# Optimization experiments

Hardware: AMD Instinct MI355X
Metric: run time of the kernel (lower is better)

## Reference

```python
import jax, jax.numpy as jnp
import numpy as np

HIDDEN = 512
LAYERS = 3
K = 8
EPS = 1e-5


def build_adjacency(coords, k):
    # squared pairwise distances (monotone in cdist, so same top-k indices)
    sq = jnp.sum(coords * coords, axis=-1)                      # [B,N]
    d2 = sq[:, :, None] + sq[:, None, :] - 2.0 * jnp.einsum('bnc,bmc->bnm', coords, coords)
    _, idx = jax.lax.top_k(-d2, k + 1)                          # smallest k+1
    idx = idx[:, :, 1:]                                         # drop self  [B,N,k]
    B, N = coords.shape[:2]
    bidx = jnp.arange(B)[:, None, None]
    ridx = jnp.arange(N)[None, :, None]
    adj = jnp.zeros((B, N, N), coords.dtype).at[bidx, ridx, idx].set(1.0)
    adj = adj + jnp.swapaxes(adj, -2, -1)                       # symmetrize
    return (adj > 0).astype(coords.dtype)


def layer_norm(x, g, b):
    mu = jnp.mean(x, axis=-1, keepdims=True)
    var = jnp.var(x, axis=-1, keepdims=True)  # biased, matches torch LayerNorm
    return (x - mu) * jax.lax.rsqrt(var + EPS) * g + b


def setup_inputs() -> dict:
    key = jax.random.key(0)
    k1, k2, k3, k4 = jax.random.split(key, 4)
    B, N, H, L = 4, 4096, HIDDEN, LAYERS
    node_features = jax.random.normal(k1, (B, N, H), dtype=jnp.float32)
    coordinates = jax.random.uniform(k2, (B, N, 2), dtype=jnp.float32)
    scale = 1.0 / np.sqrt(H)
    W = jax.random.uniform(k3, (L, H, H), dtype=jnp.float32, minval=-scale, maxval=scale)
    b = jax.random.uniform(k4, (L, H), dtype=jnp.float32, minval=-scale, maxval=scale)
    gamma = jnp.ones((L, H), dtype=jnp.float32)
    beta = jnp.zeros((L, H), dtype=jnp.float32)
    return {"node_features": node_features, "coordinates": coordinates,
            "W": W, "b": b, "gamma": gamma, "beta": beta}


def reference(node_features, coordinates, W, b, gamma, beta):
    adj = build_adjacency(coordinates, K)                       # [B,N,N]
    x = node_features
    for i in range(LAYERS):
        x_new = jnp.einsum('bnm,bmh->bnh', adj, x)              # dense aggregate
        x_new = x_new @ W[i] + b[i]                             # linear
        x_new = jax.nn.relu(layer_norm(x_new, gamma[i], beta[i]))
        x = x + x_new if i > 0 else x_new
    return x
```

## Files before the change

kernel.cpp:

```cpp
#include <hip/hip_runtime.h>
#include <stdint.h>

#define HIDDEN 512
#define NLAYERS 3
#define KNN 8
#define CAP 64
#define EPSV 1e-5f
#define GRID 32
#define NCELL (GRID * GRID)

typedef unsigned long long u64;
typedef __attribute__((ext_vector_type(8))) short short8;
typedef __attribute__((ext_vector_type(4))) float f32x4;

__device__ inline unsigned short f2bf(float x) {
  union { float f; unsigned u; } v; v.f = x;
  unsigned r = v.u + 0x7FFFu + ((v.u >> 16) & 1u);
  return (unsigned short)(r >> 16);
}
__device__ inline float bf2f(unsigned short u) {
  return __uint_as_float((unsigned)u << 16);
}

__global__ __launch_bounds__(1024) void grid_build_kernel(
    const float2* __restrict__ coords, int* __restrict__ cell_start,
    float2* __restrict__ scoord, int* __restrict__ sorig, int N) {
  __shared__ int hist[NCELL];
  __shared__ int offs[NCELL];
  int b = blockIdx.x;
  int t = threadIdx.x;
  hist[t] = 0;
  __syncthreads();
  const float2* cb = coords + (size_t)b * N;
  int mycell[4];
#pragma unroll
  for (int r = 0; r < 4; ++r) {
    int i = t + r * 1024;
    float2 c = cb[i];
    int cx = (int)(c.x * GRID); cx = cx < 0 ? 0 : (cx > GRID - 1 ? GRID - 1 : cx);
    int cy = (int)(c.y * GRID); cy = cy < 0 ? 0 : (cy > GRID - 1 ? GRID - 1 : cy);
    mycell[r] = cy * GRID + cx;
    atomicAdd(&hist[mycell[r]], 1);
  }
  __syncthreads();
  int v = hist[t];
  offs[t] = v;
  __syncthreads();
  for (int d = 1; d < NCELL; d <<= 1) {
    int add = (t >= d) ? offs[t - d] : 0;
    __syncthreads();
    offs[t] += add;
    __syncthreads();
  }
  int excl = offs[t] - v;
  cell_start[(size_t)b * (NCELL + 1) + t] = excl;
  if (t == 0) cell_start[(size_t)b * (NCELL + 1) + NCELL] = N;
  hist[t] = excl;
  __syncthreads();
#pragma unroll
  for (int r = 0; r < 4; ++r) {
    int i = t + r * 1024;
    int pos = atomicAdd(&hist[mycell[r]], 1);
    scoord[(size_t)b * N + pos] = cb[i];
    sorig[(size_t)b * N + pos] = i;
  }
}

__global__ __launch_bounds__(256) void knn_grid_kernel(
    const int* __restrict__ cell_start, const float2* __restrict__ scoord,
    const int* __restrict__ sorig, int* __restrict__ knn_s, int N, int BN) {
  int gang = (blockIdx.x * blockDim.x + threadIdx.x) >> 3;
  int sub = threadIdx.x & 7;
  if (gang >= BN) return;
  int b = gang / N;
  float2 cn = scoord[gang];
  float sqn = __fmaf_rn(cn.y, cn.y, __fmul_rn(cn.x, cn.x));
  int cx = (int)(cn.x * GRID); cx = cx < 0 ? 0 : (cx > GRID - 1 ? GRID - 1 : cx);
  int cy = (int)(cn.y * GRID); cy = cy < 0 ? 0 : (cy > GRID - 1 ? GRID - 1 : cy);
  const int* cs = cell_start + (size_t)b * (NCELL + 1);
  const float2* sc = scoord + (size_t)b * N;
  const int* so = sorig + (size_t)b * N;

  u64 list[KNN + 1];
#pragma unroll
  for (int j = 0; j <= KNN; ++j) list[j] = ~0ull;

  auto scan_cell = [&](int ux, int uy) {
    int c = uy * GRID + ux;
    int s = cs[c], e = cs[c + 1];
    for (int p = s + sub; p < e; p += 8) {
      float2 cm = sc[p];
      float sqm = __fmaf_rn(cm.y, cm.y, __fmul_rn(cm.x, cm.x));
      float dot = __fmaf_rn(cn.y, cm.y, __fmul_rn(cn.x, cm.x));
      float d2 = __fsub_rn(__fadd_rn(sqn, sqm), __fmul_rn(2.0f, dot));
      unsigned ub = __float_as_uint(d2);
      unsigned k32 = (ub & 0x80000000u) ? ~ub : (ub | 0x80000000u);
      u64 key = ((u64)k32 << 24) | ((u64)(unsigned)so[p] << 12) | (u64)(unsigned)p;
      if (key < list[KNN]) {
        u64 cur = key;
#pragma unroll
        for (int j = 0; j <= KNN; ++j) {
          u64 lo = list[j] < cur ? list[j] : cur;
          u64 hi = list[j] < cur ? cur : list[j];
          list[j] = lo;
          cur = hi;
        }
      }
    }
  };

  for (int q = 0; q <= GRID; ++q) {
    if (q == 0) {
      scan_cell(cx, cy);
    } else {
      int x0 = cx - q, x1 = cx + q, y0 = cy - q, y1 = cy + q;
      int xa = x0 < 0 ? 0 : x0, xb_ = x1 > GRID - 1 ? GRID - 1 : x1;
      for (int ux = xa; ux <= xb_; ++ux) {
        if (y0 >= 0) scan_cell(ux, y0);
        if (y1 <= GRID - 1) scan_cell(ux, y1);
      }
      int ya = (y0 + 1) < 0 ? 0 : y0 + 1, yb = (y1 - 1) > GRID - 1 ? GRID - 1 : y1 - 1;
      for (int uy = ya; uy <= yb; ++uy) {
        if (x0 >= 0) scan_cell(x0, uy);
        if (x1 <= GRID - 1) scan_cell(x1, uy);
      }
      float bound = (float)q * (1.0f / GRID);
      float thr = bound * bound - 1e-5f;
      int cntn = 0;
#pragma unroll
      for (int j = 0; j <= KNN; ++j) {
        unsigned k32 = (unsigned)(list[j] >> 24);
        float d2v = (k32 >= 0x80000000u) ? __uint_as_float(k32 & 0x7FFFFFFFu)
                                         : -__uint_as_float(~k32);
        cntn += (list[j] != ~0ull && d2v < thr) ? 1 : 0;
      }
#pragma unroll
      for (int o = 1; o < 8; o <<= 1) cntn += __shfl_xor(cntn, o, 64);
      if (cntn >= 9) break;
    }
  }

  for (int r = 0; r <= KNN; ++r) {
    u64 cand = list[0];
    u64 mn = cand;
#pragma unroll
    for (int o = 1; o < 8; o <<= 1) {
      u64 v = __shfl_xor(mn, o, 64);
      mn = v < mn ? v : mn;
    }
    if (cand == mn) {
#pragma unroll
      for (int j = 0; j < KNN; ++j) list[j] = list[j + 1];
      list[KNN] = ~0ull;
      if (r > 0) knn_s[(size_t)gang * KNN + (r - 1)] = (int)(mn & 0xFFFull);
    }
  }
}

__global__ __launch_bounds__(256) void rev_build_kernel(const int* __restrict__ knn,
                                                        int* __restrict__ cnt,
                                                        int* __restrict__ rev,
                                                        int N, int BN) {
  int e = blockIdx.x * blockDim.x + threadIdx.x;
  if (e >= BN * KNN) return;
  int bn = e >> 3;
  int m = knn[e];
  int b = bn / N;
  int gm = b * N + m;
  int pos = atomicAdd(&cnt[gm], 1);
  if (pos < CAP) rev[(size_t)gm * CAP + pos] = bn - b * N;
}

__global__ __launch_bounds__(128) void x2bf_perm_kernel(const float* __restrict__ x,
                                                        const int* __restrict__ sorig,
                                                        unsigned short* __restrict__ xs,
                                                        int N) {
  int row = blockIdx.x;
  int b = row / N;
  int src = b * N + sorig[row];
  int t = threadIdx.x;
  float4 v = ((const float4*)(x + (size_t)src * HIDDEN))[t];
  ushort4 o;
  o.x = f2bf(v.x); o.y = f2bf(v.y); o.z = f2bf(v.z); o.w = f2bf(v.w);
  ((ushort4*)(xs + (size_t)row * HIDDEN))[t] = o;
}

__global__ __launch_bounds__(128) void agg_kernel(const unsigned short* __restrict__ x,
                                                  const int* __restrict__ knn,
                                                  const int* __restrict__ cnt,
                                                  const int* __restrict__ rev,
                                                  unsigned short* __restrict__ aggb,
                                                  int N) {
  int bn = blockIdx.x;
  int b = bn / N;
  int t = threadIdx.x;
  const int* my = knn + (size_t)bn * KNN;
  int nb[KNN];
#pragma unroll
  for (int j = 0; j < KNN; ++j) nb[j] = my[j];
  const unsigned short* xb = x + (size_t)b * N * HIDDEN;
  float4 acc = {0.f, 0.f, 0.f, 0.f};
#pragma unroll
  for (int j = 0; j < KNN; ++j) {
    ushort4 v = ((const ushort4*)(xb + (size_t)nb[j] * HIDDEN))[t];
    acc.x += bf2f(v.x); acc.y += bf2f(v.y); acc.z += bf2f(v.z); acc.w += bf2f(v.w);
  }
  int indeg = cnt[bn];
  if (indeg > CAP) indeg = CAP;
  const int* rv = rev + (size_t)bn * CAP;
  for (int i = 0; i < indeg; ++i) {
    int r = rv[i];
    bool dup = false;
#pragma unroll
    for (int j = 0; j < KNN; ++j) dup = dup || (r == nb[j]);
    if (!dup) {
      ushort4 v = ((const ushort4*)(xb + (size_t)r * HIDDEN))[t];
      acc.x += bf2f(v.x); acc.y += bf2f(v.y); acc.z += bf2f(v.z); acc.w += bf2f(v.w);
    }
  }
  ushort4 o;
  o.x = f2bf(acc.x); o.y = f2bf(acc.y); o.z = f2bf(acc.z); o.w = f2bf(acc.w);
  ((ushort4*)(aggb + (size_t)bn * HIDDEN))[t] = o;
}

__global__ __launch_bounds__(256) void wconv_kernel(const float* __restrict__ W,
                                                    unsigned short* __restrict__ Wt) {
  __shared__ unsigned short tile[64][65];
  int l = blockIdx.x >> 6;
  int t6 = blockIdx.x & 63;
  int k0 = (t6 >> 3) * 64, n0 = (t6 & 7) * 64;
  const float* Wl = W + (size_t)l * HIDDEN * HIDDEN;
  unsigned short* Wtl = Wt + (size_t)l * HIDDEN * HIDDEN;
  int t = threadIdx.x;
#pragma unroll
  for (int r = 0; r < 4; ++r) {
    int row = (t >> 4) + r * 16;
    int col = (t & 15) * 4;
    float4 v = *(const float4*)(Wl + (size_t)(k0 + row) * HIDDEN + n0 + col);
    tile[col + 0][row] = f2bf(v.x);
    tile[col + 1][row] = f2bf(v.y);
    tile[col + 2][row] = f2bf(v.z);
    tile[col + 3][row] = f2bf(v.w);
  }
  __syncthreads();
#pragma unroll
  for (int r = 0; r < 4; ++r) {
    int row = (t >> 4) + r * 16;
    int col = (t & 15) * 4;
    ushort4 o;
    o.x = tile[row][col + 0]; o.y = tile[row][col + 1];
    o.z = tile[row][col + 2]; o.w = tile[row][col + 3];
    *(ushort4*)(Wtl + (size_t)(n0 + row) * HIDDEN + k0 + col) = o;
  }
}

__global__ __launch_bounds__(256) void gemm_mfma_kernel(
    const unsigned short* __restrict__ A,
    const unsigned short* __restrict__ Wt,
    const float* __restrict__ bias,
    unsigned short* __restrict__ Cb) {
  __shared__ unsigned short As[128 * 40];
  __shared__ unsigned short Bs[128 * 40];
  int t = threadIdx.x;
  int n0 = blockIdx.x * 128;
  int m0 = blockIdx.y * 128;
  int w = t >> 6, lane = t & 63;
  int wr = w >> 1, wc = w & 1;
  int lm = lane & 15, q = lane >> 4;

  f32x4 acc[4][4];
#pragma unroll
  for (int i = 0; i < 4; ++i)
#pragma unroll
    for (int j = 0; j < 4; ++j) acc[i][j] = (f32x4){0.f, 0.f, 0.f, 0.f};

  int srow = t >> 2;
  int scol = (t & 3) * 8;

  for (int k0 = 0; k0 < HIDDEN; k0 += 32) {
    uint4 a0 = *(const uint4*)(A + (size_t)(m0 + srow) * HIDDEN + k0 + scol);
    uint4 a1 = *(const uint4*)(A + (size_t)(m0 + srow + 64) * HIDDEN + k0 + scol);
    uint4 b0 = *(const uint4*)(Wt + (size_t)(n0 + srow) * HIDDEN + k0 + scol);
    uint4 b1 = *(const uint4*)(Wt + (size_t)(n0 + srow + 64) * HIDDEN + k0 + scol);
    __syncthreads();
    *(uint4*)(As + srow * 40 + scol) = a0;
    *(uint4*)(As + (srow + 64) * 40 + scol) = a1;
    *(uint4*)(Bs + srow * 40 + scol) = b0;
    *(uint4*)(Bs + (srow + 64) * 40 + scol) = b1;
    __syncthreads();
    short8 af[4], bfr[4];
#pragma unroll
    for (int i = 0; i < 4; ++i)
      af[i] = *(const short8*)(As + (wr * 64 + i * 16 + lm) * 40 + q * 8);
#pragma unroll
    for (int j = 0; j < 4; ++j)
      bfr[j] = *(const short8*)(Bs + (wc * 64 + j * 16 + lm) * 40 + q * 8);
#pragma unroll
    for (int i = 0; i < 4; ++i)
#pragma unroll
      for (int j = 0; j < 4; ++j)
        acc[i][j] = __builtin_amdgcn_mfma_f32_16x16x32_bf16(af[i], bfr[j], acc[i][j], 0, 0, 0);
  }

#pragma unroll
  for (int i = 0; i < 4; ++i) {
    int row = m0 + wr * 64 + i * 16 + q * 4;
#pragma unroll
    for (int j = 0; j < 4; ++j) {
      int col = n0 + wc * 64 + j * 16 + lm;
      float bv = bias[col];
#pragma unroll
      for (int r = 0; r < 4; ++r)
        Cb[(size_t)(row + r) * HIDDEN + col] = f2bf(acc[i][j][r] + bv);
    }
  }
}

__global__ __launch_bounds__(256) void ln_relu_res_kernel(
    const unsigned short* __restrict__ tb, const float* __restrict__ g,
    const float* __restrict__ be, unsigned short* __restrict__ xs,
    float* __restrict__ out, const int* __restrict__ sorig,
    int N, int addres, int final_) {
  int row = (blockIdx.x << 2) + (threadIdx.x >> 6);
  int lane = threadIdx.x & 63;
  uint4 u = ((const uint4*)(tb + (size_t)row * HIDDEN))[lane];
  float v[8];
  v[0] = bf2f((unsigned short)(u.x & 0xFFFFu)); v[1] = bf2f((unsigned short)(u.x >> 16));
  v[2] = bf2f((unsigned short)(u.y & 0xFFFFu)); v[3] = bf2f((unsigned short)(u.y >> 16));
  v[4] = bf2f((unsigned short)(u.z & 0xFFFFu)); v[5] = bf2f((unsigned short)(u.z >> 16));
  v[6] = bf2f((unsigned short)(u.w & 0xFFFFu)); v[7] = bf2f((unsigned short)(u.w >> 16));
  float s = 0.f, ss = 0.f;
#pragma unroll
  for (int k = 0; k < 8; ++k) { s += v[k]; ss += v[k] * v[k]; }
#pragma unroll
  for (int o = 32; o > 0; o >>= 1) {
    s += __shfl_xor(s, o, 64);
    ss += __shfl_xor(ss, o, 64);
  }
  float mu = s * (1.0f / HIDDEN);
  float var = ss * (1.0f / HIDDEN) - mu * mu;
  float inv = rsqrtf(var + EPSV);
  float4 g0 = ((const float4*)g)[2 * lane], g1 = ((const float4*)g)[2 * lane + 1];
  float4 b0 = ((const float4*)be)[2 * lane], b1 = ((const float4*)be)[2 * lane + 1];
  float gv[8] = {g0.x, g0.y, g0.z, g0.w, g1.x, g1.y, g1.z, g1.w};
  float bv[8] = {b0.x, b0.y, b0.z, b0.w, b1.x, b1.y, b1.z, b1.w};
  float o8[8];
#pragma unroll
  for (int k = 0; k < 8; ++k)
    o8[k] = fmaxf((v[k] - mu) * inv * gv[k] + bv[k], 0.f);
  ushort4* xrow = (ushort4*)(xs + (size_t)row * HIDDEN);
  if (addres) {
    ushort4 r0 = xrow[2 * lane], r1 = xrow[2 * lane + 1];
    o8[0] += bf2f(r0.x); o8[1] += bf2f(r0.y); o8[2] += bf2f(r0.z); o8[3] += bf2f(r0.w);
    o8[4] += bf2f(r1.x); o8[5] += bf2f(r1.y); o8[6] += bf2f(r1.z); o8[7] += bf2f(r1.w);
  }
  if (final_) {
    int b = row / N;
    size_t dst = (size_t)(b * N + sorig[row]) * HIDDEN;
    float4 w0 = {o8[0], o8[1], o8[2], o8[3]};
    float4 w1 = {o8[4], o8[5], o8[6], o8[7]};
    ((float4*)(out + dst))[2 * lane] = w0;
    ((float4*)(out + dst))[2 * lane + 1] = w1;
  } else {
    ushort4 q0, q1;
    q0.x = f2bf(o8[0]); q0.y = f2bf(o8[1]); q0.z = f2bf(o8[2]); q0.w = f2bf(o8[3]);
    q1.x = f2bf(o8[4]); q1.y = f2bf(o8[5]); q1.z = f2bf(o8[6]); q1.w = f2bf(o8[7]);
    xrow[2 * lane] = q0;
    xrow[2 * lane + 1] = q1;
  }
}

extern "C" void kernel_launch(void* const* d_in, const int* in_sizes, int n_in,
                              void* d_out, int out_size, void* d_ws, size_t ws_size,
                              hipStream_t stream) {
  const float* nf = (const float*)d_in[0];
  const float2* coords = (const float2*)d_in[1];
  const float* Wall = (const float*)d_in[2];
  const float* ball = (const float*)d_in[3];
  const float* gall = (const float*)d_in[4];
  const float* beall = (const float*)d_in[5];
  float* out = (float*)d_out;

  int BN = in_sizes[0] / HIDDEN;
  int N = 4096;
  int B = BN / N;

  char* ws = (char*)d_ws;
  size_t off = 0;
  auto alloc = [&](size_t bytes) -> void* {
    off = (off + 255) & ~(size_t)255;
    void* p = ws + off;
    off += bytes;
    return p;
  };
  int* knn_s = (int*)alloc((size_t)BN * KNN * sizeof(int));
  int* cnt = (int*)alloc((size_t)BN * sizeof(int));
  int* rev = (int*)alloc((size_t)BN * CAP * sizeof(int));
  unsigned short* aggb = (unsigned short*)alloc((size_t)BN * HIDDEN * sizeof(unsigned short));
  unsigned short* tmpb = (unsigned short*)alloc((size_t)BN * HIDDEN * sizeof(unsigned short));
  unsigned short* Wt = (unsigned short*)alloc((size_t)NLAYERS * HIDDEN * HIDDEN * sizeof(unsigned short));
  unsigned short* xs = (unsigned short*)alloc((size_t)BN * HIDDEN * sizeof(unsigned short));
  int* cell_start = (int*)alloc((size_t)B * (NCELL + 1) * sizeof(int));
  float2* scoord = (float2*)alloc((size_t)BN * sizeof(float2));
  int* sorig = (int*)alloc((size_t)BN * sizeof(int));

  hipMemsetAsync(cnt, 0, (size_t)BN * sizeof(int), stream);
  grid_build_kernel<<<B, 1024, 0, stream>>>(coords, cell_start, scoord, sorig, N);
  knn_grid_kernel<<<(BN * 8 + 255) / 256, 256, 0, stream>>>(cell_start, scoord, sorig, knn_s, N, BN);
  rev_build_kernel<<<(BN * KNN) / 256, 256, 0, stream>>>(knn_s, cnt, rev, N, BN);
  wconv_kernel<<<NLAYERS * 64, 256, 0, stream>>>(Wall, Wt);
  x2bf_perm_kernel<<<BN, 128, 0, stream>>>(nf, sorig, xs, N);

  for (int l = 0; l < NLAYERS; ++l) {
    agg_kernel<<<BN, 128, 0, stream>>>(xs, knn_s, cnt, rev, aggb, N);
    gemm_mfma_kernel<<<dim3(HIDDEN / 128, BN / 128), 256, 0, stream>>>(
        aggb, Wt + (size_t)l * HIDDEN * HIDDEN, ball + (size_t)l * HIDDEN, tmpb);
    ln_relu_res_kernel<<<BN / 4, 256, 0, stream>>>(
        tmpb, gall + (size_t)l * HIDDEN, beall + (size_t)l * HIDDEN,
        xs, out, sorig, N, l > 0, l == NLAYERS - 1);
  }
}
```

Measured before the change: 286.7 us.

## Fuse reverse-edge build into kNN kernel and stage GEMM tiles via global_load_lds

The reverse adjacency construction (atomic count and rev list) moves into the kNN selection loop, which removes one kernel launch and the re-read of the kNN index array. Separately, the MFMA GEMM now copies A and W tiles straight from global memory into LDS with global_load_lds, skipping the register round trip, and drops the row padding to a 32-element stride. The unpadded layout may bring LDS bank conflicts on the fragment reads, and the load is still not double-buffered.

After: 282.6 us. Within noise of the previous version (-1.4%).

```diff
diff --git a/kernel.cpp b/kernel.cpp
--- a/kernel.cpp
+++ b/kernel.cpp
@@ -12,6 +12,11 @@
 typedef unsigned long long u64;
 typedef __attribute__((ext_vector_type(8))) short short8;
 typedef __attribute__((ext_vector_type(4))) float f32x4;
+
+#define GLL16(gp, lp)                                                         \
+  __builtin_amdgcn_global_load_lds(                                           \
+      (const __attribute__((address_space(1))) unsigned int*)(gp),            \
+      (__attribute__((address_space(3))) unsigned int*)(lp), 16, 0, 0)
 
 __device__ inline unsigned short f2bf(float x) {
   union { float f; unsigned u; } v; v.f = x;
@@ -68,7 +73,8 @@
 
 __global__ __launch_bounds__(256) void knn_grid_kernel(
     const int* __restrict__ cell_start, const float2* __restrict__ scoord,
-    const int* __restrict__ sorig, int* __restrict__ knn_s, int N, int BN) {
+    const int* __restrict__ sorig, int* __restrict__ knn_s,
+    int* __restrict__ cnt, int* __restrict__ rev, int N, int BN) {
   int gang = (blockIdx.x * blockDim.x + threadIdx.x) >> 3;
   int sub = threadIdx.x & 7;
   if (gang >= BN) return;
@@ -140,6 +146,7 @@
     }
   }
 
+  int gl = gang - b * N;
   for (int r = 0; r <= KNN; ++r) {
     u64 cand = list[0];
     u64 mn = cand;
@@ -152,23 +159,15 @@
 #pragma unroll
       for (int j = 0; j < KNN; ++j) list[j] = list[j + 1];
       list[KNN] = ~0ull;
-      if (r > 0) knn_s[(size_t)gang * KNN + (r - 1)] = (int)(mn & 0xFFFull);
-    }
-  }
-}
-
-__global__ __launch_bounds__(256) void rev_build_kernel(const int* __restrict__ knn,
-                                                        int* __restrict__ cnt,
-                                                        int* __restrict__ rev,
-                                                        int N, int BN) {
-  int e = blockIdx.x * blockDim.x + threadIdx.x;
-  if (e >= BN * KNN) return;
-  int bn = e >> 3;
-  int m = knn[e];
-  int b = bn / N;
-  int gm = b * N + m;
-  int pos = atomicAdd(&cnt[gm], 1);
-  if (pos < CAP) rev[(size_t)gm * CAP + pos] = bn - b * N;
+      if (r > 0) {
+        int m = (int)(mn & 0xFFFull);
+        knn_s[(size_t)gang * KNN + (r - 1)] = m;
+        int gm = b * N + m;
+        int pos = atomicAdd(&cnt[gm], 1);
+        if (pos < CAP) rev[(size_t)gm * CAP + pos] = gl;
+      }
+    }
+  }
 }
 
 __global__ __launch_bounds__(128) void x2bf_perm_kernel(const float* __restrict__ x,
@@ -259,8 +258,8 @@
     const unsigned short* __restrict__ Wt,
     const float* __restrict__ bias,
     unsigned short* __restrict__ Cb) {
-  __shared__ unsigned short As[128 * 40];
-  __shared__ unsigned short Bs[128 * 40];
+  __shared__ unsigned short As[128 * 32];
+  __shared__ unsigned short Bs[128 * 32];
   int t = threadIdx.x;
   int n0 = blockIdx.x * 128;
   int m0 = blockIdx.y * 128;
@@ -274,27 +273,29 @@
 #pragma unroll
     for (int j = 0; j < 4; ++j) acc[i][j] = (f32x4){0.f, 0.f, 0.f, 0.f};
 
-  int srow = t >> 2;
-  int scol = (t & 3) * 8;
+  int lrow = lane >> 2;
+  int lcol = (lane & 3) * 8;
+  int e0 = w, e1 = w + 4;
+
+  const unsigned short* Arow0 = A + (size_t)(m0 + e0 * 16 + lrow) * HIDDEN + lcol;
+  const unsigned short* Arow1 = A + (size_t)(m0 + e1 * 16 + lrow) * HIDDEN + lcol;
+  const unsigned short* Brow0 = Wt + (size_t)(n0 + e0 * 16 + lrow) * HIDDEN + lcol;
+  const unsigned short* Brow1 = Wt + (size_t)(n0 + e1 * 16 + lrow) * HIDDEN + lcol;
 
   for (int k0 = 0; k0 < HIDDEN; k0 += 32) {
-    uint4 a0 = *(const uint4*)(A + (size_t)(m0 + srow) * HIDDEN + k0 + scol);
-    uint4 a1 = *(const uint4*)(A + (size_t)(m0 + srow + 64) * HIDDEN + k0 + scol);
-    uint4 b0 = *(const uint4*)(Wt + (size_t)(n0 + srow) * HIDDEN + k0 + scol);
-    uint4 b1 = *(const uint4*)(Wt + (size_t)(n0 + srow + 64) * HIDDEN + k0 + scol);
     __syncthreads();
-    *(uint4*)(As + srow * 40 + scol) = a0;
-    *(uint4*)(As + (srow + 64) * 40 + scol) = a1;
-    *(uint4*)(Bs + srow * 40 + scol) = b0;
-    *(uint4*)(Bs + (srow + 64) * 40 + scol) = b1;
+    GLL16(Arow0 + k0, As + e0 * 16 * 32);
+    GLL16(Arow1 + k0, As + e1 * 16 * 32);
+    GLL16(Brow0 + k0, Bs + e0 * 16 * 32);
+    GLL16(Brow1 + k0, Bs + e1 * 16 * 32);
     __syncthreads();
     short8 af[4], bfr[4];
 #pragma unroll
     for (int i = 0; i < 4; ++i)
-      af[i] = *(const short8*)(As + (wr * 64 + i * 16 + lm) * 40 + q * 8);
+      af[i] = *(const short8*)(As + (wr * 64 + i * 16 + lm) * 32 + q * 8);
 #pragma unroll
     for (int j = 0; j < 4; ++j)
-      bfr[j] = *(const short8*)(Bs + (wc * 64 + j * 16 + lm) * 40 + q * 8);
+      bfr[j] = *(const short8*)(Bs + (wc * 64 + j * 16 + lm) * 32 + q * 8);
 #pragma unroll
     for (int i = 0; i < 4; ++i)
 #pragma unroll
@@ -406,8 +407,7 @@
 
   hipMemsetAsync(cnt, 0, (size_t)BN * sizeof(int), stream);
   grid_build_kernel<<<B, 1024, 0, stream>>>(coords, cell_start, scoord, sorig, N);
-  knn_grid_kernel<<<(BN * 8 + 255) / 256, 256, 0, stream>>>(cell_start, scoord, sorig, knn_s, N, BN);
-  rev_build_kernel<<<(BN * KNN) / 256, 256, 0, stream>>>(knn_s, cnt, rev, N, BN);
+  knn_grid_kernel<<<(BN * 8 + 255) / 256, 256, 0, stream>>>(cell_start, scoord, sorig, knn_s, cnt, rev, N, BN);
   wconv_kernel<<<NLAYERS * 64, 256, 0, stream>>>(Wall, Wt);
   x2bf_perm_kernel<<<BN, 128, 0, stream>>>(nf, sorig, xs, N);
 
```
